# Kernel tuning notes

Hardware: AMD Instinct MI355X
Metric: run time of the kernel (lower is better)

The kernel has to match this reference:

```python
import jax, jax.numpy as jnp
import numpy as np

H = 20          # hidden_size
IN = 2          # GRU input / l1 output dim


def setup_inputs() -> dict:
    key = jax.random.key(0)
    ks = jax.random.split(key, 7)
    B = 32768
    s = 1.0 / np.sqrt(H)  # torch default init scale
    hidden = jax.random.normal(ks[0], (1, B, H), dtype=jnp.float32)
    w_ih = jax.random.uniform(ks[1], (3 * H, IN), jnp.float32, -s, s)
    w_hh = jax.random.uniform(ks[2], (3 * H, H), jnp.float32, -s, s)
    b_ih = jax.random.uniform(ks[3], (3 * H,), jnp.float32, -s, s)
    b_hh = jax.random.uniform(ks[4], (3 * H,), jnp.float32, -s, s)
    w_l = jax.random.uniform(ks[5], (IN, H), jnp.float32, -s, s)
    b_l = jax.random.uniform(ks[6], (IN,), jnp.float32, -s, s)
    return {"hidden": hidden, "w_ih": w_ih, "w_hh": w_hh,
            "b_ih": b_ih, "b_hh": b_hh, "w_l": w_l, "b_l": b_l,
            "step": 200}


def reference(hidden, w_ih, w_hh, b_ih, b_hh, w_l, b_l, step):
    reverse = True
    B = hidden.shape[1]
    h0 = hidden[0]                      # [B, H]
    x0 = jnp.zeros((B, IN), hidden.dtype)  # first GRU input is zeros

    def gru_step(carry, _):
        h, x = carry
        gi = x @ w_ih.T + b_ih          # [B, 3H]
        gh = h @ w_hh.T + b_hh          # [B, 3H]
        ir, iz, inn = jnp.split(gi, 3, axis=-1)
        hr, hz, hn = jnp.split(gh, 3, axis=-1)
        r = jax.nn.sigmoid(ir + hr)
        z = jax.nn.sigmoid(iz + hz)
        n = jnp.tanh(inn + r * hn)
        h_new = (1.0 - z) * n + z * h   # [B, H]
        y = h_new @ w_l.T + b_l         # [B, 2] -> next input
        return (h_new, y), y

    (_, _), ys = jax.lax.scan(gru_step, (h0, x0), None, length=step)
    # ys: [step, B, 2]; original appends per-step then reverses the list
    if reverse:
        ys = ys[::-1]
    return jnp.transpose(ys, (1, 0, 2))  # [B, step, 2]
```

## Files before the change

### kernel.cpp

```cpp
#include <hip/hip_runtime.h>

#define HDIM 20
#define BLOCK 256

typedef __fp16 half8 __attribute__((ext_vector_type(8)));
typedef float  float4v __attribute__((ext_vector_type(4)));

static __device__ __forceinline__ float4v mfma16(half8 a, half8 b, float4v c) {
    return __builtin_amdgcn_mfma_f32_16x16x32_f16(a, b, c, 0, 0, 0);
}


__global__ __launch_bounds__(BLOCK, 2) void gru_decoder_kernel(
    const float* __restrict__ hidden,
    const float* __restrict__ w_ih,
    const float* __restrict__ w_hh,
    const float* __restrict__ b_ih,
    const float* __restrict__ b_hh,
    const float* __restrict__ w_l,
    const float* __restrict__ b_l,
    const int*  __restrict__ step_ptr,
    float* __restrict__ out,
    int B)
{
    __shared__ __align__(16) __fp16 lds[4 * 16 * 40];

    const int tid = threadIdx.x;
    const int l   = tid & 63;
    const int wv  = tid >> 6;
    const int el  = l & 15;
    const int q   = l >> 4;
    const int e   = (blockIdx.x * 4 + wv) * 16 + el;
    const int step = *step_ptr;

    const int i_t = el & 3;
    const int qr  = el >> 2;
    const int k0  = 8 * q;

    half8 Afold[5], Azero[5], Ay;
    #pragma unroll
    for (int T = 0; T < 5; ++T) {
        const int u  = 4 * T + qr;
        const int rr = (i_t == 0) ? u : (i_t == 1) ? 20 + u : 40 + u;
        half8 hf, h0;
        #pragma unroll
        for (int j = 0; j < 8; ++j) {
            const int k = k0 + j;
            float a_f = 0.f, a_0 = 0.f;
            if (k < HDIM) {
                float wxv = w_ih[rr * 2 + 0] * w_l[k] + w_ih[rr * 2 + 1] * w_l[HDIM + k];
                float whv = w_hh[rr * HDIM + k];
                if (i_t <= 1)      { a_f = whv + wxv; a_0 = whv; }
                else if (i_t == 2) { a_f = wxv;       a_0 = 0.f; }
                else               { a_f = whv;       a_0 = whv; }
            } else if (k == HDIM) {
                float bx = w_ih[rr * 2 + 0] * b_l[0] + w_ih[rr * 2 + 1] * b_l[1];
                if (i_t <= 1)      { a_f = b_ih[rr] + b_hh[rr] + bx; a_0 = b_ih[rr] + b_hh[rr]; }
                else if (i_t == 2) { a_f = b_ih[rr] + bx;            a_0 = b_ih[rr]; }
                else               { a_f = b_hh[rr];                 a_0 = b_hh[rr]; }
            }
            hf[j] = (__fp16)a_f;
            h0[j] = (__fp16)a_0;
        }
        Afold[T] = hf;
        Azero[T] = h0;
    }
    {
        half8 hy;
        #pragma unroll
        for (int j = 0; j < 8; ++j) {
            const int k = k0 + j;
            float v = 0.f;
            if (el < 2) {
                if (k < HDIM)       v = w_l[el * HDIM + k];
                else if (k == HDIM) v = b_l[el];
            }
            hy[j] = (__fp16)v;
        }
        Ay = hy;
    }

    __fp16* elhp = &lds[(wv * 16 + el) * 40];
    float hprev[5];
    {
        const float* hb = hidden + (size_t)e * HDIM;
        #pragma unroll
        for (int T = 0; T < 5; ++T) {
            float hv = hb[4 * T + q];
            hprev[T] = hv;
            elhp[4 * T + q] = (__fp16)hv;
        }
        if (q == 2) {
            elhp[20] = (__fp16)1.f; elhp[21] = (__fp16)0.f;
            elhp[22] = (__fp16)0.f; elhp[23] = (__fp16)0.f;
        }
        if (q == 3) {
            half8 z8 = {};
            *(half8*)(elhp + 24) = z8;
        }
    }
    half8 Bf = *(const half8*)(elhp + 8 * q);

    const float NLOG2E   = -1.4426950408889634f;
    const float TWOLOG2E =  2.8853900817779268f;

    auto do_step = [&](const half8* A) {
        float4v z4 = {0.f, 0.f, 0.f, 0.f};
        float4v C[5];
        #pragma unroll
        for (int T = 0; T < 5; ++T) C[T] = mfma16(A[T], Bf, z4);
        #pragma unroll
        for (int T = 0; T < 5; ++T) {
            float ar = C[T][0], az = C[T][1], anI = C[T][2], anH = C[T][3];
            float r = __builtin_amdgcn_rcpf(1.f + __builtin_amdgcn_exp2f(ar * NLOG2E));
            float z = __builtin_amdgcn_rcpf(1.f + __builtin_amdgcn_exp2f(az * NLOG2E));
            float npre = anI + r * anH;
            float n = 1.f - 2.f * __builtin_amdgcn_rcpf(1.f + __builtin_amdgcn_exp2f(npre * TWOLOG2E));
            float hv = n + z * (hprev[T] - n);
            hprev[T] = hv;
            elhp[4 * T + q] = (__fp16)hv;
        }
        Bf = *(const half8*)(elhp + 8 * q);
    };

    float* outp = out + (size_t)e * 2 * step;

    do_step(Azero);
    for (int t = 1; t < step; ++t) {
        float4v z4 = {0.f, 0.f, 0.f, 0.f};
        float4v cy = mfma16(Ay, Bf, z4);
        if (q == 0) {
            float2 st; st.x = cy[0]; st.y = cy[1];
            *(float2*)(outp + 2 * (step - t)) = st;
        }
        do_step(Afold);
    }
    {
        float4v z4 = {0.f, 0.f, 0.f, 0.f};
        float4v cy = mfma16(Ay, Bf, z4);
        if (q == 0) {
            float2 st; st.x = cy[0]; st.y = cy[1];
            *(float2*)(outp + 0) = st;
        }
    }
}

extern "C" void kernel_launch(void* const* d_in, const int* in_sizes, int n_in,
                              void* d_out, int out_size, void* d_ws, size_t ws_size,
                              hipStream_t stream) {
    const float* hidden = (const float*)d_in[0];
    const float* w_ih   = (const float*)d_in[1];
    const float* w_hh   = (const float*)d_in[2];
    const float* b_ih   = (const float*)d_in[3];
    const float* b_hh   = (const float*)d_in[4];
    const float* w_l    = (const float*)d_in[5];
    const float* b_l    = (const float*)d_in[6];
    const int*   step   = (const int*)d_in[7];
    float* out = (float*)d_out;

    int B = in_sizes[0] / HDIM;
    int grid = B / 64;

    gru_decoder_kernel<<<grid, BLOCK, 0, stream>>>(
        hidden, w_ih, w_hh, b_ih, b_hh, w_l, b_l, step, out, B);
}
```

Before: 188.4 us.

## Permute K layout so each lane owns its B slice; fold exp scales into weights

```diff
diff --git a/kernel.cpp b/kernel.cpp
--- a/kernel.cpp
+++ b/kernel.cpp
@@ -33,34 +33,37 @@
     const int e   = (blockIdx.x * 4 + wv) * 16 + el;
     const int step = *step_ptr;
 
-    const int i_t = el & 3;
-    const int qr  = el >> 2;
-    const int k0  = 8 * q;
+    const float NL2E = -1.4426950408889634f;
+    const float T2L2E = 2.8853900817779268f;
+
+    const int u_dst = el >> 2;
+    const int g     = el & 3;
 
     half8 Afold[5], Azero[5], Ay;
     #pragma unroll
     for (int T = 0; T < 5; ++T) {
-        const int u  = 4 * T + qr;
-        const int rr = (i_t == 0) ? u : (i_t == 1) ? 20 + u : 40 + u;
+        const int u  = 4 * T + u_dst;
+        const int rr = (g == 0) ? u : (g == 1) ? 20 + u : 40 + u;
+        const float sc = (g <= 1) ? NL2E : T2L2E;
         half8 hf, h0;
         #pragma unroll
         for (int j = 0; j < 8; ++j) {
-            const int k = k0 + j;
-            float a_f = 0.f, a_0 = 0.f;
-            if (k < HDIM) {
-                float wxv = w_ih[rr * 2 + 0] * w_l[k] + w_ih[rr * 2 + 1] * w_l[HDIM + k];
-                float whv = w_hh[rr * HDIM + k];
-                if (i_t <= 1)      { a_f = whv + wxv; a_0 = whv; }
-                else if (i_t == 2) { a_f = wxv;       a_0 = 0.f; }
-                else               { a_f = whv;       a_0 = whv; }
-            } else if (k == HDIM) {
+            float af = 0.f, a0 = 0.f;
+            if (j < 5) {
+                const int uk = 4 * j + q;
+                float wx = w_ih[rr * 2 + 0] * w_l[uk] + w_ih[rr * 2 + 1] * w_l[HDIM + uk];
+                float wh = w_hh[rr * HDIM + uk];
+                if (g <= 1)      { af = wh + wx; a0 = wh; }
+                else if (g == 2) { af = wx;      a0 = 0.f; }
+                else             { af = wh;      a0 = wh; }
+            } else if (j == 7 && q == 0) {
                 float bx = w_ih[rr * 2 + 0] * b_l[0] + w_ih[rr * 2 + 1] * b_l[1];
-                if (i_t <= 1)      { a_f = b_ih[rr] + b_hh[rr] + bx; a_0 = b_ih[rr] + b_hh[rr]; }
-                else if (i_t == 2) { a_f = b_ih[rr] + bx;            a_0 = b_ih[rr]; }
-                else               { a_f = b_hh[rr];                 a_0 = b_hh[rr]; }
+                if (g <= 1)      { af = b_ih[rr] + b_hh[rr] + bx; a0 = b_ih[rr] + b_hh[rr]; }
+                else if (g == 2) { af = b_ih[rr] + bx;            a0 = b_ih[rr]; }
+                else             { af = b_hh[rr];                 a0 = b_hh[rr]; }
             }
-            hf[j] = (__fp16)a_f;
-            h0[j] = (__fp16)a_0;
+            hf[j] = (__fp16)(af * sc);
+            h0[j] = (__fp16)(a0 * sc);
         }
         Afold[T] = hf;
         Azero[T] = h0;
@@ -69,66 +72,66 @@
         half8 hy;
         #pragma unroll
         for (int j = 0; j < 8; ++j) {
-            const int k = k0 + j;
             float v = 0.f;
             if (el < 2) {
-                if (k < HDIM)       v = w_l[el * HDIM + k];
-                else if (k == HDIM) v = b_l[el];
+                if (j < 5)                   v = w_l[el * HDIM + 4 * j + q];
+                else if (j == 7 && q == 0)   v = b_l[el];
             }
             hy[j] = (__fp16)v;
         }
         Ay = hy;
     }
 
-    __fp16* elhp = &lds[(wv * 16 + el) * 40];
+    __fp16* slice = &lds[(wv * 16 + el) * 40 + 8 * q];
     float hprev[5];
+    half8 Bf;
     {
         const float* hb = hidden + (size_t)e * HDIM;
+        half8 b0;
         #pragma unroll
         for (int T = 0; T < 5; ++T) {
             float hv = hb[4 * T + q];
             hprev[T] = hv;
-            elhp[4 * T + q] = (__fp16)hv;
+            b0[T] = (__fp16)hv;
         }
-        if (q == 2) {
-            elhp[20] = (__fp16)1.f; elhp[21] = (__fp16)0.f;
-            elhp[22] = (__fp16)0.f; elhp[23] = (__fp16)0.f;
-        }
-        if (q == 3) {
-            half8 z8 = {};
-            *(half8*)(elhp + 24) = z8;
-        }
+        b0[5] = (__fp16)0.f;
+        b0[6] = (__fp16)0.f;
+        b0[7] = (__fp16)((q == 0) ? 1.f : 0.f);
+        *(half8*)slice = b0;
+        Bf = b0;
     }
-    half8 Bf = *(const half8*)(elhp + 8 * q);
 
-    const float NLOG2E   = -1.4426950408889634f;
-    const float TWOLOG2E =  2.8853900817779268f;
+    const float4v czero = {0.f, 0.f, 0.f, 0.f};
+    typedef __fp16 half2v __attribute__((ext_vector_type(2)));
+    typedef float  float2v __attribute__((ext_vector_type(2)));
 
     auto do_step = [&](const half8* A) {
-        float4v z4 = {0.f, 0.f, 0.f, 0.f};
         float4v C[5];
         #pragma unroll
-        for (int T = 0; T < 5; ++T) C[T] = mfma16(A[T], Bf, z4);
+        for (int T = 0; T < 5; ++T) C[T] = mfma16(A[T], Bf, czero);
         #pragma unroll
         for (int T = 0; T < 5; ++T) {
-            float ar = C[T][0], az = C[T][1], anI = C[T][2], anH = C[T][3];
-            float r = __builtin_amdgcn_rcpf(1.f + __builtin_amdgcn_exp2f(ar * NLOG2E));
-            float z = __builtin_amdgcn_rcpf(1.f + __builtin_amdgcn_exp2f(az * NLOG2E));
-            float npre = anI + r * anH;
-            float n = 1.f - 2.f * __builtin_amdgcn_rcpf(1.f + __builtin_amdgcn_exp2f(npre * TWOLOG2E));
-            float hv = n + z * (hprev[T] - n);
+            float r = __builtin_amdgcn_rcpf(1.f + __builtin_amdgcn_exp2f(C[T][0]));
+            float z = __builtin_amdgcn_rcpf(1.f + __builtin_amdgcn_exp2f(C[T][1]));
+            float npre2 = C[T][2] + r * C[T][3];
+            float tn = __builtin_amdgcn_rcpf(1.f + __builtin_amdgcn_exp2f(npre2));
+            float n = __builtin_fmaf(-2.f, tn, 1.f);
+            float hv = __builtin_fmaf(z, hprev[T] - n, n);
             hprev[T] = hv;
-            elhp[4 * T + q] = (__fp16)hv;
         }
-        Bf = *(const half8*)(elhp + 8 * q);
+        half2v p01 = __builtin_amdgcn_cvt_pkrtz(hprev[0], hprev[1]);
+        half2v p23 = __builtin_amdgcn_cvt_pkrtz(hprev[2], hprev[3]);
+        float2v d2; d2[0] = __builtin_bit_cast(float, p01); d2[1] = __builtin_bit_cast(float, p23);
+        *(float2v*)slice = d2;
+        slice[4] = (__fp16)hprev[4];
+        Bf = *(const half8*)slice;
     };
 
     float* outp = out + (size_t)e * 2 * step;
 
     do_step(Azero);
     for (int t = 1; t < step; ++t) {
-        float4v z4 = {0.f, 0.f, 0.f, 0.f};
-        float4v cy = mfma16(Ay, Bf, z4);
+        float4v cy = mfma16(Ay, Bf, czero);
         if (q == 0) {
             float2 st; st.x = cy[0]; st.y = cy[1];
             *(float2*)(outp + 2 * (step - t)) = st;
@@ -136,8 +139,7 @@
         do_step(Afold);
     }
     {
-        float4v z4 = {0.f, 0.f, 0.f, 0.f};
-        float4v cy = mfma16(Ay, Bf, z4);
+        float4v cy = mfma16(Ay, Bf, czero);
         if (q == 0) {
             float2 st; st.x = cy[0]; st.y = cy[1];
             *(float2*)(outp + 0) = st;
```

Result: faster. 171.5 us (-9.0%).
